# Performance work log

Measured on AMD Instinct MI355X. Metric: run time of the kernel, lower is better.

The kernel has to match this reference:

```python
import jax, jax.numpy as jnp
import numpy as np
import math

LMAX = 2
S = (LMAX + 1) ** 2
N_ATOMS = 32000
N_FEAT = 128


def _cg(j1, m1, j2, m2, j3, m3):
    # Clebsch-Gordan coefficient <j1 m1 j2 m2 | j3 m3> via the Racah formula.
    if m3 != m1 + m2 or not (abs(j1 - j2) <= j3 <= j1 + j2):
        return 0.0
    f = math.factorial
    pre = math.sqrt((2 * j3 + 1) * f(j3 + j1 - j2) * f(j3 - j1 + j2) * f(j1 + j2 - j3) / f(j1 + j2 + j3 + 1))
    pre *= math.sqrt(f(j3 + m3) * f(j3 - m3) * f(j1 - m1) * f(j1 + m1) * f(j2 - m2) * f(j2 + m2))
    kmin = max(0, j2 - j3 - m1, j1 - j3 + m2)
    kmax = min(j1 + j2 - j3, j1 - m1, j2 + m2)
    s = 0.0
    for k in range(kmin, kmax + 1):
        s += (-1) ** k / (f(k) * f(j1 + j2 - j3 - k) * f(j1 - m1 - k) * f(j2 + m2 - k) * f(j3 - j2 + m1 + k) * f(j3 - j1 - m2 + k))
    return pre * s


def _build_sparse_cg(lmax):
    # Mirrors schnetpack generate_clebsch_gordan_rsh + nonzero extraction in __init__.
    ls = np.arange(lmax + 1)
    lidx = np.repeat(ls, 2 * ls + 1)
    midx = np.concatenate([np.arange(-l, l + 1) for l in ls])
    n = lidx.shape[0]
    cg = np.zeros((n, n, n))
    for i in range(n):
        for j in range(n):
            for k in range(n):
                cg[i, j, k] = _cg(int(lidx[i]), int(midx[i]), int(lidx[j]), int(midx[j]), int(lidx[k]), int(midx[k]))
    # complex -> real spherical-harmonic unitary change of basis
    U = np.zeros((n, n), dtype=np.complex128)
    off = 0
    for l in ls:
        for m in range(-l, l + 1):
            r = off + l + m
            if m == 0:
                U[r, off + l] = 1.0
            elif m > 0:
                U[r, off + l - m] = 1.0 / np.sqrt(2.0)
                U[r, off + l + m] = (-1.0) ** m / np.sqrt(2.0)
            else:
                am = -m
                U[r, off + l + m] = 1j / np.sqrt(2.0)
                U[r, off + l + am] = -((-1.0) ** am) * 1j / np.sqrt(2.0)
        off += 2 * int(l) + 1
    cg_rsh = np.einsum('ijk,ai,bj,ck->abc', cg.astype(np.complex128), U, U, U.conj())
    parity = (-1.0) ** lidx
    pmask = (parity[:, None, None] * parity[None, :, None]) == parity[None, None, :]
    cg_rsh = np.real(cg_rsh) * pmask
    cg_rsh[np.abs(cg_rsh) < 1e-9] = 0.0
    idx = np.argwhere(cg_rsh != 0.0)
    idx_1, idx_2, idx_out = idx[:, 0], idx[:, 1], idx[:, 2]
    vals = cg_rsh[idx_1, idx_2, idx_out].astype(np.float32)
    return idx_1, idx_2, idx_out, vals, lidx


def setup_inputs() -> dict:
    key = jax.random.key(0)
    k_x, k_w = jax.random.split(key)
    idx_1, idx_2, idx_out, cg_vals, lidx = _build_sparse_cg(LMAX)
    x = jax.random.normal(k_x, (N_ATOMS, S, N_FEAT), dtype=jnp.float32)
    # kaiming_uniform_(a=sqrt(5)) on (lmax+1, lmax+1): bound = 1/sqrt(fan_in)
    bound = 1.0 / math.sqrt(LMAX + 1)
    weight = jax.random.uniform(k_w, (LMAX + 1, LMAX + 1), minval=-bound, maxval=bound, dtype=jnp.float32)
    return {
        "x": x,
        "weight": weight,
        "cg_vals": jnp.asarray(cg_vals),
        "idx_1": jnp.asarray(idx_1, dtype=jnp.int32),
        "idx_2": jnp.asarray(idx_2, dtype=jnp.int32),
        "idx_out": jnp.asarray(idx_out, dtype=jnp.int32),
        "widx_1": jnp.asarray(lidx[idx_1], dtype=jnp.int32),
        "widx_2": jnp.asarray(lidx[idx_2], dtype=jnp.int32),
    }


def reference(x, weight, cg_vals, idx_1, idx_2, idx_out, widx_1, widx_2):
    # y[n, s, f] = sum_{s1,s2} x[n,s1,f] x[n,s2,f] W[l(s1),l(s2)] C[s1,s2,s]
    Wcg = weight[widx_1, widx_2] * cg_vals            # [nnz]
    temp = x[:, idx_1, :] * x[:, idx_2, :] * Wcg[None, :, None]  # [N, nnz, F]
    y = jnp.zeros_like(x).at[:, idx_out, :].add(temp)            # scatter-add over dim 1 -> [N, S, F]
    return y
```

## Files before the change

### kernel.cpp

```cpp
#include <hip/hip_runtime.h>


#define S9 9
#define NFEAT 128
#define ATOMS_PER_BLOCK 8
#define THREADS 256
#define ROW_BYTES (THREADS * 16)


__global__ void so3_prep_kernel(const float* __restrict__ weight,
                                const float* __restrict__ cg_vals,
                                const int* __restrict__ idx_1,
                                const int* __restrict__ idx_2,
                                const int* __restrict__ idx_out,
                                const int* __restrict__ widx_1,
                                const int* __restrict__ widx_2,
                                int nnz, int* __restrict__ ws) {
    __shared__ float d[S9 * 81];
    __shared__ int   segs[S9 + 1];
    const int tid = threadIdx.x;

    for (int i = tid; i < S9 * 81; i += THREADS) d[i] = 0.f;
    __syncthreads();

    for (int e = tid; e < nnz; e += THREADS) {
        const int i = idx_1[e];
        const int j = idx_2[e];
        const int k = idx_out[e];
        const float w = weight[widx_1[e] * 3 + widx_2[e]] * cg_vals[e];
        const int a = min(i, j);
        const int b = max(i, j);
        atomicAdd(&d[k * 81 + a * 9 + b], w);
    }
    __syncthreads();

    if (tid == 0) {
        int pos = 0;
        for (int k = 0; k < S9; ++k) {
            segs[k] = pos;
            int c = 0;
            for (int a = 0; a < S9; ++a)
                for (int b = a; b < S9; ++b)
                    if (d[k * 81 + a * 9 + b] != 0.f) ++c;
            pos += (c + 3) & ~3;
        }
        segs[S9] = pos;
        for (int k = 0; k <= S9; ++k) ws[k] = segs[k];
    }
    __syncthreads();

    if (tid < S9) {
        const int k = tid;
        uint2* tab = (uint2*)(ws + 32);
        int pos = segs[k];
        for (int a = 0; a < S9; ++a)
            for (int b = a; b < S9; ++b) {
                const float v = d[k * 81 + a * 9 + b];
                if (v != 0.f) {
                    uint2 t;
                    t.x = (unsigned)(a * ROW_BYTES) | ((unsigned)(b * ROW_BYTES) << 16);
                    t.y = __float_as_uint(v);
                    tab[pos++] = t;
                }
            }
        for (; pos < segs[k + 1]; ++pos) tab[pos] = make_uint2(0u, 0u);
    }
}

__global__ __launch_bounds__(THREADS) void so3_main_kernel(
        const float* __restrict__ x,
        const int* __restrict__ ws,
        float* __restrict__ y) {
    __shared__ __align__(16) float xs[S9 * THREADS * 4];

    const int tid  = threadIdx.x;
    const int atom = blockIdx.x * ATOMS_PER_BLOCK + (tid >> 5);
    const int c4   = tid & 31;
    const size_t rowBase = (size_t)atom * S9 * NFEAT + (size_t)c4 * 4;

    #pragma unroll
    for (int s = 0; s < S9; ++s) {
        const float* src = x + rowBase + (size_t)s * NFEAT;
        float* dst = &xs[s * (THREADS * 4) + tid * 4];
        __builtin_amdgcn_global_load_lds(
            (const __attribute__((address_space(1))) unsigned int*)src,
            (__attribute__((address_space(3))) unsigned int*)dst,
            16, 0, 0);
    }
    __syncthreads();

    const char* base = (const char*)xs + tid * 16;
    const uint2* __restrict__ tab = (const uint2*)(ws + 32);

    #pragma unroll
    for (int k = 0; k < S9; ++k) {
        float4 acc = make_float4(0.f, 0.f, 0.f, 0.f);
        const int eBeg = __builtin_amdgcn_readfirstlane(ws[k]);
        const int eEnd = __builtin_amdgcn_readfirstlane(ws[k + 1]);
        for (int e = eBeg; e < eEnd; e += 4) {
            #pragma unroll
            for (int u = 0; u < 4; ++u) {
                const uint2 t = tab[e + u];
                const float4 a4 = *reinterpret_cast<const float4*>(base + (t.x & 0xFFFFu));
                const float4 b4 = *reinterpret_cast<const float4*>(base + (t.x >> 16));
                const float w = __uint_as_float(t.y);
                acc.x = fmaf(w * a4.x, b4.x, acc.x);
                acc.y = fmaf(w * a4.y, b4.y, acc.y);
                acc.z = fmaf(w * a4.z, b4.z, acc.z);
                acc.w = fmaf(w * a4.w, b4.w, acc.w);
            }
        }
        *reinterpret_cast<float4*>(y + rowBase + (size_t)k * NFEAT) = acc;
    }
}

extern "C" void kernel_launch(void* const* d_in, const int* in_sizes, int n_in,
                              void* d_out, int out_size, void* d_ws, size_t ws_size,
                              hipStream_t stream) {
    const float* x       = (const float*)d_in[0];
    const float* weight  = (const float*)d_in[1];
    const float* cg_vals = (const float*)d_in[2];
    const int* idx_1     = (const int*)d_in[3];
    const int* idx_2     = (const int*)d_in[4];
    const int* idx_out   = (const int*)d_in[5];
    const int* widx_1    = (const int*)d_in[6];
    const int* widx_2    = (const int*)d_in[7];
    float* y             = (float*)d_out;
    int* ws              = (int*)d_ws;

    const int nnz     = in_sizes[2];
    const int n_atoms = in_sizes[0] / (S9 * NFEAT);

    so3_prep_kernel<<<1, THREADS, 0, stream>>>(weight, cg_vals, idx_1, idx_2,
                                               idx_out, widx_1, widx_2, nnz, ws);

    const int grid = n_atoms / ATOMS_PER_BLOCK;
    so3_main_kernel<<<grid, THREADS, 0, stream>>>(x, ws, y);
}
```

Measured before the change: 64.19 us.

## Compute symmetric pair products once in registers with a dense pair-by-output weight table

Drops the LDS staging and the per-output sparse table walk. Each thread now loads its 9 float4 rows into registers, forms each used symmetric pair product once, and accumulates it into all 9 outputs through a dense 45x9 weight table guarded by a wave-uniform bitmask. Outputs are written with nontemporal stores. This removes the LDS traffic and the indirect offset decoding, but adds zero-weight FMAs, more registers and scalar weight loads per pair.

```diff
diff --git a/kernel.cpp b/kernel.cpp
--- a/kernel.cpp
+++ b/kernel.cpp
@@ -3,9 +3,10 @@
 
 #define S9 9
 #define NFEAT 128
-#define ATOMS_PER_BLOCK 8
 #define THREADS 256
-#define ROW_BYTES (THREADS * 16)
+#define NPAIR 45
+
+typedef float f4 __attribute__((ext_vector_type(4)));
 
 
 __global__ void so3_prep_kernel(const float* __restrict__ weight,
@@ -16,11 +17,12 @@
                                 const int* __restrict__ widx_1,
                                 const int* __restrict__ widx_2,
                                 int nnz, int* __restrict__ ws) {
-    __shared__ float d[S9 * 81];
-    __shared__ int   segs[S9 + 1];
+    __shared__ float d[NPAIR * S9];
+    __shared__ unsigned long long smask;
     const int tid = threadIdx.x;
 
-    for (int i = tid; i < S9 * 81; i += THREADS) d[i] = 0.f;
+    for (int i = tid; i < NPAIR * S9; i += THREADS) d[i] = 0.f;
+    if (tid == 0) smask = 0ull;
     __syncthreads();
 
     for (int e = tid; e < nnz; e += THREADS) {
@@ -30,88 +32,66 @@
         const float w = weight[widx_1[e] * 3 + widx_2[e]] * cg_vals[e];
         const int a = min(i, j);
         const int b = max(i, j);
-        atomicAdd(&d[k * 81 + a * 9 + b], w);
+        const int p = a * 9 - a * (a - 1) / 2 + (b - a);
+        atomicAdd(&d[p * S9 + k], w);
     }
     __syncthreads();
 
-    if (tid == 0) {
-        int pos = 0;
-        for (int k = 0; k < S9; ++k) {
-            segs[k] = pos;
-            int c = 0;
-            for (int a = 0; a < S9; ++a)
-                for (int b = a; b < S9; ++b)
-                    if (d[k * 81 + a * 9 + b] != 0.f) ++c;
-            pos += (c + 3) & ~3;
-        }
-        segs[S9] = pos;
-        for (int k = 0; k <= S9; ++k) ws[k] = segs[k];
+    if (tid < NPAIR) {
+        bool any = false;
+        for (int k = 0; k < S9; ++k) any |= (d[tid * S9 + k] != 0.f);
+        if (any) atomicOr(&smask, 1ull << tid);
     }
     __syncthreads();
 
-    if (tid < S9) {
-        const int k = tid;
-        uint2* tab = (uint2*)(ws + 32);
-        int pos = segs[k];
-        for (int a = 0; a < S9; ++a)
-            for (int b = a; b < S9; ++b) {
-                const float v = d[k * 81 + a * 9 + b];
-                if (v != 0.f) {
-                    uint2 t;
-                    t.x = (unsigned)(a * ROW_BYTES) | ((unsigned)(b * ROW_BYTES) << 16);
-                    t.y = __float_as_uint(v);
-                    tab[pos++] = t;
-                }
-            }
-        for (; pos < segs[k + 1]; ++pos) tab[pos] = make_uint2(0u, 0u);
-    }
+    if (tid == 0) *(unsigned long long*)ws = smask;
+    float* W = (float*)(ws + 8);
+    for (int i = tid; i < NPAIR * S9; i += THREADS) W[i] = d[i];
 }
 
 __global__ __launch_bounds__(THREADS) void so3_main_kernel(
         const float* __restrict__ x,
         const int* __restrict__ ws,
         float* __restrict__ y) {
-    __shared__ __align__(16) float xs[S9 * THREADS * 4];
+    const int gid  = blockIdx.x * THREADS + threadIdx.x;
+    const int atom = gid >> 5;
+    const int c4   = gid & 31;
+    const size_t base = (size_t)atom * (S9 * NFEAT) + (size_t)c4 * 4;
 
-    const int tid  = threadIdx.x;
-    const int atom = blockIdx.x * ATOMS_PER_BLOCK + (tid >> 5);
-    const int c4   = tid & 31;
-    const size_t rowBase = (size_t)atom * S9 * NFEAT + (size_t)c4 * 4;
+    const unsigned long long mask = *(const unsigned long long*)ws;
+    const float* __restrict__ W = (const float*)(ws + 8);
+
+    f4 xv[S9];
+    #pragma unroll
+    for (int s = 0; s < S9; ++s)
+        xv[s] = *(const f4*)(x + base + (size_t)s * NFEAT);
+
+    f4 acc[S9];
+    #pragma unroll
+    for (int k = 0; k < S9; ++k) acc[k] = (f4)0.f;
 
     #pragma unroll
-    for (int s = 0; s < S9; ++s) {
-        const float* src = x + rowBase + (size_t)s * NFEAT;
-        float* dst = &xs[s * (THREADS * 4) + tid * 4];
-        __builtin_amdgcn_global_load_lds(
-            (const __attribute__((address_space(1))) unsigned int*)src,
-            (__attribute__((address_space(3))) unsigned int*)dst,
-            16, 0, 0);
+    for (int a = 0; a < S9; ++a) {
+        #pragma unroll
+        for (int b = a; b < S9; ++b) {
+            const int p = a * 9 - a * (a - 1) / 2 + (b - a);
+            if (mask & (1ull << p)) {
+                const f4 prod = xv[a] * xv[b];
+                #pragma unroll
+                for (int k = 0; k < S9; ++k) {
+                    const float w = W[p * S9 + k];
+                    acc[k][0] = fmaf(w, prod[0], acc[k][0]);
+                    acc[k][1] = fmaf(w, prod[1], acc[k][1]);
+                    acc[k][2] = fmaf(w, prod[2], acc[k][2]);
+                    acc[k][3] = fmaf(w, prod[3], acc[k][3]);
+                }
+            }
+        }
     }
-    __syncthreads();
-
-    const char* base = (const char*)xs + tid * 16;
-    const uint2* __restrict__ tab = (const uint2*)(ws + 32);
 
     #pragma unroll
-    for (int k = 0; k < S9; ++k) {
-        float4 acc = make_float4(0.f, 0.f, 0.f, 0.f);
-        const int eBeg = __builtin_amdgcn_readfirstlane(ws[k]);
-        const int eEnd = __builtin_amdgcn_readfirstlane(ws[k + 1]);
-        for (int e = eBeg; e < eEnd; e += 4) {
-            #pragma unroll
-            for (int u = 0; u < 4; ++u) {
-                const uint2 t = tab[e + u];
-                const float4 a4 = *reinterpret_cast<const float4*>(base + (t.x & 0xFFFFu));
-                const float4 b4 = *reinterpret_cast<const float4*>(base + (t.x >> 16));
-                const float w = __uint_as_float(t.y);
-                acc.x = fmaf(w * a4.x, b4.x, acc.x);
-                acc.y = fmaf(w * a4.y, b4.y, acc.y);
-                acc.z = fmaf(w * a4.z, b4.z, acc.z);
-                acc.w = fmaf(w * a4.w, b4.w, acc.w);
-            }
-        }
-        *reinterpret_cast<float4*>(y + rowBase + (size_t)k * NFEAT) = acc;
-    }
+    for (int k = 0; k < S9; ++k)
+        __builtin_nontemporal_store(acc[k], (f4*)(y + base + (size_t)k * NFEAT));
 }
 
 extern "C" void kernel_launch(void* const* d_in, const int* in_sizes, int n_in,
@@ -134,6 +114,6 @@
     so3_prep_kernel<<<1, THREADS, 0, stream>>>(weight, cg_vals, idx_1, idx_2,
                                                idx_out, widx_1, widx_2, nnz, ws);
 
-    const int grid = n_atoms / ATOMS_PER_BLOCK;
-    so3_main_kernel<<<grid, THREADS, 0, stream>>>(x, ws, y);
+    const int total = n_atoms * 32;
+    so3_main_kernel<<<total / THREADS, THREADS, 0, stream>>>(x, ws, y);
 }
```

Result: slower. 66.59 us (+3.7%).
